# Kernel optimization log

Hardware: AMD Instinct MI355X
Metric: run time of the kernel (lower is better)

## Reference

```python
import jax, jax.numpy as jnp
import numpy as np

SMOOTH = 1.0
MAX_DIST = 10


def _neighbor_conv(x):
    # 3x3 ones kernel with zero center, padding=1 (NCHW, C=1)
    k = jnp.ones((1, 1, 3, 3), x.dtype).at[0, 0, 1, 1].set(0.0)
    return jax.lax.conv_general_dilated(
        x, k, window_strides=(1, 1), padding=[(1, 1), (1, 1)],
        dimension_numbers=('NCHW', 'OIHW', 'NCHW'))


def _analyze_skeleton(skel):
    n = _neighbor_conv(skel)
    on = skel > 0.5
    endpoints = ((n == 1) & on).astype(skel.dtype)
    midpoints = ((n == 2) & on).astype(skel.dtype)
    junctions = ((n > 2) & on).astype(skel.dtype)
    return endpoints, midpoints, junctions


def _iou(p, g):
    inter = jnp.sum(p * g, axis=(2, 3))
    union = jnp.sum(p, axis=(2, 3)) + jnp.sum(g, axis=(2, 3)) - inter
    return (inter + SMOOTH) / (union + SMOOTH)


def _structural_similarity(pred_skel, gt_skel):
    pe, pm, pj = _analyze_skeleton(pred_skel)
    ge, gm, gj = _analyze_skeleton(gt_skel)
    e_iou, m_iou, j_iou = _iou(pe, ge), _iou(pm, gm), _iou(pj, gj)
    ge_c = jnp.sum(ge, axis=(2, 3))
    gj_c = jnp.sum(gj, axis=(2, 3))
    gm_c = jnp.sum(gm, axis=(2, 3))
    total = ge_c + gj_c + gm_c + SMOOTH
    loss = 1.0 - ((ge_c / total) * e_iou + (gj_c / total) * j_iou + (gm_c / total) * m_iou)
    return loss.mean()


def _maxpool3(x):
    return jax.lax.reduce_window(
        x, -jnp.inf, jax.lax.max,
        window_dimensions=(1, 1, 3, 3), window_strides=(1, 1, 1, 1),
        padding=[(0, 0), (0, 0), (1, 1), (1, 1)])


def _distance_approximation(target, reference):
    # Fixed MAX_DIST iterations; identical math to the torch early-exit loop
    # because new_points requires ~found_mask (no distance is overwritten).
    tgt_on = target > 0.5

    def step(carry, d):
        dilated, found, dist = carry
        dilated = _maxpool3(dilated)
        new = (dilated > 0.5) & tgt_on & (~found)
        dist = dist + d.astype(dist.dtype) * new.astype(dist.dtype)
        return (dilated, found | new, dist), None

    init = (reference, jnp.zeros(target.shape, bool), jnp.zeros_like(target))
    (_, found, dist), _ = jax.lax.scan(step, init, jnp.arange(1, MAX_DIST + 1, dtype=jnp.int32))
    unfound = tgt_on & (~found)
    dist = dist + jnp.asarray(MAX_DIST, dist.dtype) * unfound.astype(dist.dtype)
    total_points = jnp.sum(tgt_on.astype(dist.dtype), axis=(2, 3))
    return jnp.sum(dist, axis=(2, 3)) / (total_points + SMOOTH)


def _medial_axis_distance(pred_skel, gt_skel):
    p2g = _distance_approximation(pred_skel, gt_skel)
    g2p = _distance_approximation(gt_skel, pred_skel)
    return (((p2g + g2p) / 2.0) / MAX_DIST).mean()


def setup_inputs() -> dict:
    key = jax.random.key(0)
    k1, k2 = jax.random.split(key)
    B, C, H, W = 32, 1, 512, 512
    pred_skel = jax.random.uniform(k1, (B, C, H, W), dtype=jnp.float32)
    gt_skel = (jax.random.uniform(k2, (B, C, H, W), dtype=jnp.float32) < 0.1).astype(jnp.float32)
    return {"pred_skel": pred_skel, "gt_skel": gt_skel}


def reference(pred_skel, gt_skel):
    inter = jnp.sum(pred_skel * gt_skel, axis=(2, 3))
    psum = jnp.sum(pred_skel, axis=(2, 3))
    gsum = jnp.sum(gt_skel, axis=(2, 3))
    dice = (2.0 * inter + SMOOTH) / (psum + gsum + SMOOTH)
    dice_loss = 1.0 - dice.mean()
    structural_loss = _structural_similarity(pred_skel, gt_skel)
    medial_loss = _medial_axis_distance(pred_skel, gt_skel)
    avg_mag = (dice_loss + structural_loss + medial_loss) / 3.0
    bal_dice = dice_loss / (dice_loss + SMOOTH) * avg_mag
    bal_struct = structural_loss / (structural_loss + SMOOTH) * avg_mag
    bal_medial = medial_loss / (medial_loss + SMOOTH) * avg_mag
    return bal_dice + bal_struct + bal_medial
```

## Files before the change

### kernel.cpp

```cpp
#include <hip/hip_runtime.h>
#include <stdint.h>

#define BATCH 32
#define H 512
#define W 512
#define NACC 16
#define TH 32
#define HALO 9
#define RH (TH + 2*HALO)
#define NWORDS (RH*8)
#define NT 512
#define NW (NT/64)
#define NTILE (H/TH)
#define NBLK (NTILE*BATCH)


__global__ __launch_bounds__(NT, 4) void fused_kernel(
    const float* __restrict__ pred, const float* __restrict__ gt,
    float* __restrict__ part)
{
    __shared__ uint64_t MpS[NWORDS + 2];
    __shared__ uint64_t MgS[NWORDS + 2];
    __shared__ float    EC[2][TH];
    __shared__ float    red[NW][16];

    uint64_t* Mp = MpS + 1;
    uint64_t* Mg = MgS + 1;

    int fid  = blockIdx.x;
    int b    = fid & 31;
    int tile = fid >> 5;

    const float* pimg = pred + (size_t)b * H * W;
    const float* gimg = gt   + (size_t)b * H * W;
    int y0 = tile * TH;
    int tid = threadIdx.x, lane = tid & 63, wid = tid >> 6;

    for (int s = wid; s < NWORDS; s += 2 * NW) {
        int sB = s + NW;
        int ryA = y0 - HALO + (s >> 3);
        int ryB = y0 - HALO + (sB >> 3);
        float vpA = 0.f, vgA = 0.f, vpB = 0.f, vgB = 0.f;
        if ((unsigned)ryA < (unsigned)H) {
            int i0 = ryA * W + (s & 7) * 64 + lane;
            vpA = pimg[i0]; vgA = gimg[i0];
        }
        if ((unsigned)ryB < (unsigned)H) {
            int i1 = ryB * W + (sB & 7) * 64 + lane;
            vpB = pimg[i1]; vgB = gimg[i1];
        }
        unsigned long long mpA = __ballot(vpA > 0.5f);
        unsigned long long mgA = __ballot(vgA > 0.5f);
        unsigned long long mpB = __ballot(vpB > 0.5f);
        unsigned long long mgB = __ballot(vgB > 0.5f);
        if (lane == 0) {
            Mp[s]  = mpA; Mg[s]  = mgA;
            Mp[sB] = mpB; Mg[sB] = mgB;
        }
    }
    if (tid == 0) { MpS[0] = 0; MpS[NWORDS + 1] = 0; MgS[0] = 0; MgS[NWORDS + 1] = 0; }
    if (tid < 2 * TH) {
        int c = tid >> 5, r = tid & (TH - 1);
        int y = y0 + r, col = 255 + c;
        float sum = (y > 0     ? pimg[(size_t)(y - 1) * W + col] : 0.f)
                  +              pimg[(size_t)y * W + col]
                  + (y < H - 1 ? pimg[(size_t)(y + 1) * W + col] : 0.f);
        EC[c][r] = sum;
    }
    __syncthreads();

    float v0 = 0.f, v1 = 0.f;
    uint64_t cpack = 0ULL;
    {
        int qi = tid & 127, h = tid >> 7;
        int x4 = qi * 4;
        int wdx = qi >> 4;
        int ss = (qi & 15) * 4;
        int ys = y0 + h * 8;

        auto win6 = [&](int rb) -> uint32_t {
            const uint64_t* row = &Mg[rb * 8];
            uint64_t bm = row[wdx];
            if (ss == 0) {
                uint64_t lo = wdx ? row[wdx - 1] : 0ULL;
                return (uint32_t)(((bm << 1) | (lo >> 63)) & 0x3FULL);
            }
            uint32_t v = (uint32_t)((bm >> (ss - 1)) & 0x3FULL);
            if (ss == 60) {
                uint64_t hi = (wdx < 7) ? row[wdx + 1] : 0ULL;
                v |= ((uint32_t)hi & 1u) << 5;
            }
            return v;
        };

        int rb0 = h * 8 + HALO - 1;
        uint32_t wU = win6(rb0), wM = win6(rb0 + 1);

        float4 pm4, pc4;
        {
            bool hm = ys > 0;
            pm4 = hm ? *(const float4*)(pimg + (size_t)(ys - 1) * W + x4)
                     : make_float4(0, 0, 0, 0);
            pc4 = *(const float4*)(pimg + (size_t)ys * W + x4);
        }
        for (int r = 0; r < 8; ++r) {
            int y = ys + r;
            float4 pp4 = (y < H - 1) ? *(const float4*)(pimg + (size_t)(y + 1) * W + x4)
                                     : make_float4(0, 0, 0, 0);
            uint32_t wD = win6(rb0 + 2 + r);
            int ry = h * 8 + r;

            float ps[6];
            ps[1] = pm4.x + pc4.x + pp4.x; ps[2] = pm4.y + pc4.y + pp4.y;
            ps[3] = pm4.z + pc4.z + pp4.z; ps[4] = pm4.w + pc4.w + pp4.w;
            float psl = __shfl_up(ps[4], 1, 64);
            float psr = __shfl_down(ps[1], 1, 64);
            if (lane == 0)  psl = (qi == 0)   ? 0.f : EC[0][ry];
            if (lane == 63) psr = (qi == 127) ? 0.f : EC[1][ry];
            ps[0] = psl; ps[5] = psr;

            float pcv[4] = {pc4.x, pc4.y, pc4.z, pc4.w};
            #pragma unroll
            for (int j = 0; j < 4; ++j) {
                float np = ps[j] + ps[j + 1] + ps[j + 2] - pcv[j];
                bool pon = pcv[j] > 0.5f;
                bool pe  = pon && (np == 1.f);
                bool pmb = pon && (np == 2.f);
                bool pjb = pon && (np > 2.f);
                uint32_t n9 = ((wU >> j) & 7u) | (((wM >> j) & 7u) << 3) | (((wD >> j) & 7u) << 6);
                uint32_t cen = (wM >> (j + 1)) & 1u;
                int ng = __popc(n9) - (int)cen;
                bool gon = cen != 0u;
                bool ge  = gon && (ng == 1);
                bool gmb = gon && (ng == 2);
                bool gjb = gon && (ng > 2);
                v1 += pcv[j];
                v0 += gon ? pcv[j] : 0.f;
                cpack += (uint64_t)pe
                       | ((uint64_t)pmb << 7)
                       | ((uint64_t)pjb << 14)
                       | ((uint64_t)ge  << 21)
                       | ((uint64_t)gmb << 28)
                       | ((uint64_t)gjb << 35)
                       | ((uint64_t)(pe  && ge)  << 42)
                       | ((uint64_t)(pmb && gmb) << 49)
                       | ((uint64_t)(pjb && gjb) << 56);
            }
            pm4 = pc4; pc4 = pp4; wU = wM; wM = wD;
        }
    }

    bool isP = tid < 256;
    int idx = tid & 255;
    int o   = (HALO + (idx >> 3)) * 8 + (idx & 7);
    int w   = idx & 7;
    bool wL = (w > 0), wR = (w < 7);
    const uint64_t* MT = isP ? Mp : Mg;
    const uint64_t* MV = isP ? Mg : Mp;

    uint64_t T = MT[o];
    int dcnt = __popcll(T);
    int dsum = dcnt;
    uint64_t VM = MV[o];
    uint64_t VL = wL ? MV[o - 1] : 0ULL;
    uint64_t VR = wR ? MV[o + 1] : 0ULL;
    uint64_t C = VM;

    #pragma unroll
    for (int a = 1; a <= 9; ++a) {
        int lo = o - 8 * a, hi = o + 8 * a;
        uint64_t NM = MV[lo] | MV[hi];
        uint64_t NL = wL ? (MV[lo - 1] | MV[hi - 1]) : 0ULL;
        uint64_t NR = wR ? (MV[lo + 1] | MV[hi + 1]) : 0ULL;
        uint64_t SL = NL, SM = NM, SR = NR;
        const int m = a - 1;
        if (m >= 1) {
            SM |= (SM << 1) | (SM >> 1) | (SL >> 63) | (SR << 63);
            SL |= SL << 1; SR |= SR >> 1;
        }
        if (m >= 2) {
            const int s = (m == 2) ? 1 : 2;
            SM |= (SM << s) | (SM >> s) | (SL >> (64 - s)) | (SR << (64 - s));
            SL |= SL << s; SR |= SR >> s;
        }
        if (m >= 4) {
            const int s = (m - 3 < 4) ? (m - 3) : 4;
            SM |= (SM << s) | (SM >> s) | (SL >> (64 - s)) | (SR << (64 - s));
            SL |= SL << s; SR |= SR >> s;
        }
        if (m >= 8) {
            const int s = m - 7;
            SM |= (SM << s) | (SM >> s) | (SL >> (64 - s)) | (SR << (64 - s));
            SL |= SL << s; SR |= SR >> s;
        }
        C |= SM;
        VL |= NL; VM |= NM; VR |= NR;
        C |= (VM << a) | (VM >> a) | (VL >> (64 - a)) | (VR << (64 - a));
        dsum += __popcll(T & ~C);
    }

    float vals[16];
    vals[0] = v0; vals[1] = v1;
    vals[2]  = isP ? 0.f : (float)dcnt;
    vals[3]  = (float)((cpack      ) & 0x7F);
    vals[4]  = (float)((cpack >> 7 ) & 0x7F);
    vals[5]  = (float)((cpack >> 14) & 0x7F);
    vals[6]  = (float)((cpack >> 21) & 0x7F);
    vals[7]  = (float)((cpack >> 28) & 0x7F);
    vals[8]  = (float)((cpack >> 35) & 0x7F);
    vals[9]  = (float)((cpack >> 42) & 0x7F);
    vals[10] = (float)((cpack >> 49) & 0x7F);
    vals[11] = (float)((cpack >> 56) & 0x7F);
    vals[12] = isP ? (float)dsum : 0.f;
    vals[13] = isP ? (float)dcnt : 0.f;
    vals[14] = isP ? 0.f : (float)dsum;
    vals[15] = isP ? 0.f : (float)dcnt;
    #pragma unroll
    for (int j = 0; j < 16; ++j)
        #pragma unroll
        for (int off = 32; off; off >>= 1)
            vals[j] += __shfl_down(vals[j], off, 64);
    if (lane == 0) {
        #pragma unroll
        for (int j = 0; j < 16; ++j) red[wid][j] = vals[j];
    }
    __syncthreads();
    if (tid < 16) {
        float s = 0.f;
        #pragma unroll
        for (int wv = 0; wv < NW; ++wv) s += red[wv][tid];
        part[fid * NACC + tid] = s;
    }
}

__global__ __launch_bounds__(512) void final_kernel(
    const float* __restrict__ part, float* __restrict__ out)
{
    __shared__ float sacc[BATCH][NACC];
    __shared__ float tri[BATCH][3];
    int t = threadIdx.x;
    {
        int b = t >> 4, k = t & 15;
        float s = 0.f;
        #pragma unroll 4
        for (int j = 0; j < NTILE; ++j)
            s += part[((j << 5) + b) * NACC + k];
        sacc[b][k] = s;
    }
    __syncthreads();
    if (t < BATCH) {
        const float* a = sacc[t];
        float inter = a[0], psum = a[1], gsum = a[2];
        float dice = (2.f * inter + 1.f) / (psum + gsum + 1.f);

        float pe = a[3], pm = a[4], pj = a[5];
        float ge = a[6], gm = a[7], gj = a[8];
        float ie = a[9], im = a[10], ij = a[11];
        float e_iou = (ie + 1.f) / (pe + ge - ie + 1.f);
        float m_iou = (im + 1.f) / (pm + gm - im + 1.f);
        float j_iou = (ij + 1.f) / (pj + gj - ij + 1.f);
        float total = ge + gj + gm + 1.f;
        float sloss = 1.f - ((ge / total) * e_iou + (gj / total) * j_iou + (gm / total) * m_iou);

        float p2g = a[12] / (a[13] + 1.f);
        float g2p = a[14] / (a[15] + 1.f);
        float med = ((p2g + g2p) * 0.5f) / 10.f;
        tri[t][0] = dice; tri[t][1] = sloss; tri[t][2] = med;
    }
    __syncthreads();
    if (t == 0) {
        float dice = 0.f, sloss = 0.f, med = 0.f;
        for (int b = 0; b < BATCH; ++b) {
            dice += tri[b][0]; sloss += tri[b][1]; med += tri[b][2];
        }
        float dice_loss  = 1.f - dice / (float)BATCH;
        float structural = sloss / (float)BATCH;
        float medial     = med / (float)BATCH;
        float avg = (dice_loss + structural + medial) / 3.f;
        float r = dice_loss  / (dice_loss  + 1.f) * avg
                + structural / (structural + 1.f) * avg
                + medial     / (medial     + 1.f) * avg;
        out[0] = r;
    }
}

extern "C" void kernel_launch(void* const* d_in, const int* in_sizes, int n_in,
                              void* d_out, int out_size, void* d_ws, size_t ws_size,
                              hipStream_t stream)
{
    const float* pred = (const float*)d_in[0];
    const float* gt   = (const float*)d_in[1];
    float* part = (float*)d_ws;
    float* out  = (float*)d_out;

    fused_kernel<<<dim3(NBLK), NT, 0, stream>>>(pred, gt, part);
    final_kernel<<<1, 512, 0, stream>>>(part, out);
}
```

Before: 126.5 us.

## Double block size, split stencil into pre-sync pred pass and post-sync GT pass

Raises threads per block to 1024 so each thread handles 4 rows instead of 8. The pred-neighbour stencil, which only reads global memory, now runs before the barrier, which overlaps it with the shared bitmask build. The dice sums move into the bitmask load loop, and the edge-column sums come from per-lane loads instead of a shared EC array. Flags are packed as 3-bit fields and counted with popcount masks. Only half the threads run the distance loop, and the larger block may cut occupancy and raise register pressure.

Result: slower. 167.9 us (+32.7%).

```diff
diff --git a/kernel.cpp b/kernel.cpp
--- a/kernel.cpp
+++ b/kernel.cpp
@@ -9,7 +9,7 @@
 #define HALO 9
 #define RH (TH + 2*HALO)
 #define NWORDS (RH*8)
-#define NT 512
+#define NT 1024
 #define NW (NT/64)
 #define NTILE (H/TH)
 #define NBLK (NTILE*BATCH)
@@ -21,7 +21,6 @@
 {
     __shared__ uint64_t MpS[NWORDS + 2];
     __shared__ uint64_t MgS[NWORDS + 2];
-    __shared__ float    EC[2][TH];
     __shared__ float    red[NW][16];
 
     uint64_t* Mp = MpS + 1;
@@ -36,48 +35,89 @@
     int y0 = tile * TH;
     int tid = threadIdx.x, lane = tid & 63, wid = tid >> 6;
 
+    float v0 = 0.f, v1 = 0.f;
     for (int s = wid; s < NWORDS; s += 2 * NW) {
         int sB = s + NW;
-        int ryA = y0 - HALO + (s >> 3);
-        int ryB = y0 - HALO + (sB >> 3);
+        bool okB = sB < NWORDS;
+        int rA = s >> 3, rB = sB >> 3;
+        int ryA = y0 - HALO + rA, ryB = y0 - HALO + rB;
         float vpA = 0.f, vgA = 0.f, vpB = 0.f, vgB = 0.f;
         if ((unsigned)ryA < (unsigned)H) {
             int i0 = ryA * W + (s & 7) * 64 + lane;
             vpA = pimg[i0]; vgA = gimg[i0];
         }
-        if ((unsigned)ryB < (unsigned)H) {
+        if (okB && (unsigned)ryB < (unsigned)H) {
             int i1 = ryB * W + (sB & 7) * 64 + lane;
             vpB = pimg[i1]; vgB = gimg[i1];
         }
         unsigned long long mpA = __ballot(vpA > 0.5f);
         unsigned long long mgA = __ballot(vgA > 0.5f);
-        unsigned long long mpB = __ballot(vpB > 0.5f);
-        unsigned long long mgB = __ballot(vgB > 0.5f);
-        if (lane == 0) {
-            Mp[s]  = mpA; Mg[s]  = mgA;
-            Mp[sB] = mpB; Mg[sB] = mgB;
+        if (lane == 0) { Mp[s] = mpA; Mg[s] = mgA; }
+        if (rA >= HALO && rA < HALO + TH) { v1 += vpA; v0 += (vgA > 0.5f) ? vpA : 0.f; }
+        if (okB) {
+            unsigned long long mpB = __ballot(vpB > 0.5f);
+            unsigned long long mgB = __ballot(vgB > 0.5f);
+            if (lane == 0) { Mp[sB] = mpB; Mg[sB] = mgB; }
+            if (rB >= HALO && rB < HALO + TH) { v1 += vpB; v0 += (vgB > 0.5f) ? vpB : 0.f; }
         }
     }
     if (tid == 0) { MpS[0] = 0; MpS[NWORDS + 1] = 0; MgS[0] = 0; MgS[NWORDS + 1] = 0; }
-    if (tid < 2 * TH) {
-        int c = tid >> 5, r = tid & (TH - 1);
-        int y = y0 + r, col = 255 + c;
-        float sum = (y > 0     ? pimg[(size_t)(y - 1) * W + col] : 0.f)
-                  +              pimg[(size_t)y * W + col]
-                  + (y < H - 1 ? pimg[(size_t)(y + 1) * W + col] : 0.f);
-        EC[c][r] = sum;
-    }
-    __syncthreads();
-
-    float v0 = 0.f, v1 = 0.f;
-    uint64_t cpack = 0ULL;
+
+    uint64_t ppack = 0ULL;
     {
         int qi = tid & 127, h = tid >> 7;
         int x4 = qi * 4;
+        int ys = y0 + h * 4;
+        bool needL = (lane == 0)  && (qi == 64);
+        bool needR = (lane == 63) && (qi == 63);
+        bool needE = needL || needR;
+        int ecol = needL ? 255 : 256;
+        float em = 0.f, ec = 0.f;
+        if (needE) {
+            if (ys > 0) em = pimg[(size_t)(ys - 1) * W + ecol];
+            ec = pimg[(size_t)ys * W + ecol];
+        }
+        float4 pm4 = (ys > 0) ? *(const float4*)(pimg + (size_t)(ys - 1) * W + x4)
+                              : make_float4(0, 0, 0, 0);
+        float4 pc4 = *(const float4*)(pimg + (size_t)ys * W + x4);
+        #pragma unroll
+        for (int r = 0; r < 4; ++r) {
+            int y = ys + r;
+            float4 pp4 = (y < H - 1) ? *(const float4*)(pimg + (size_t)(y + 1) * W + x4)
+                                     : make_float4(0, 0, 0, 0);
+            float ep = 0.f;
+            if (needE && y < H - 1) ep = pimg[(size_t)(y + 1) * W + ecol];
+            float ecs = em + ec + ep;
+
+            float ps[6];
+            ps[1] = pm4.x + pc4.x + pp4.x; ps[2] = pm4.y + pc4.y + pp4.y;
+            ps[3] = pm4.z + pc4.z + pp4.z; ps[4] = pm4.w + pc4.w + pp4.w;
+            float psl = __shfl_up(ps[4], 1, 64);
+            float psr = __shfl_down(ps[1], 1, 64);
+            if (lane == 0)  psl = needL ? ecs : 0.f;
+            if (lane == 63) psr = needR ? ecs : 0.f;
+            ps[0] = psl; ps[5] = psr;
+
+            float pcv[4] = {pc4.x, pc4.y, pc4.z, pc4.w};
+            #pragma unroll
+            for (int j = 0; j < 4; ++j) {
+                float np = ps[j] + ps[j + 1] + ps[j + 2] - pcv[j];
+                bool pon = pcv[j] > 0.5f;
+                uint32_t f = (uint32_t)(pon && (np == 1.f))
+                           | ((uint32_t)(pon && (np == 2.f)) << 1)
+                           | ((uint32_t)(pon && (np > 2.f))  << 2);
+                ppack |= (uint64_t)f << (3 * (r * 4 + j));
+            }
+            pm4 = pc4; pc4 = pp4; em = ec; ec = ep;
+        }
+    }
+    __syncthreads();
+
+    uint64_t gpack = 0ULL;
+    {
+        int qi = tid & 127, h = tid >> 7;
         int wdx = qi >> 4;
         int ss = (qi & 15) * 4;
-        int ys = y0 + h * 8;
-
         auto win6 = [&](int rb) -> uint32_t {
             const uint64_t* row = &Mg[rb * 8];
             uint64_t bm = row[wdx];
@@ -92,129 +132,97 @@
             }
             return v;
         };
-
-        int rb0 = h * 8 + HALO - 1;
+        int rb0 = h * 4 + HALO - 1;
         uint32_t wU = win6(rb0), wM = win6(rb0 + 1);
-
-        float4 pm4, pc4;
-        {
-            bool hm = ys > 0;
-            pm4 = hm ? *(const float4*)(pimg + (size_t)(ys - 1) * W + x4)
-                     : make_float4(0, 0, 0, 0);
-            pc4 = *(const float4*)(pimg + (size_t)ys * W + x4);
-        }
-        for (int r = 0; r < 8; ++r) {
-            int y = ys + r;
-            float4 pp4 = (y < H - 1) ? *(const float4*)(pimg + (size_t)(y + 1) * W + x4)
-                                     : make_float4(0, 0, 0, 0);
+        #pragma unroll
+        for (int r = 0; r < 4; ++r) {
             uint32_t wD = win6(rb0 + 2 + r);
-            int ry = h * 8 + r;
-
-            float ps[6];
-            ps[1] = pm4.x + pc4.x + pp4.x; ps[2] = pm4.y + pc4.y + pp4.y;
-            ps[3] = pm4.z + pc4.z + pp4.z; ps[4] = pm4.w + pc4.w + pp4.w;
-            float psl = __shfl_up(ps[4], 1, 64);
-            float psr = __shfl_down(ps[1], 1, 64);
-            if (lane == 0)  psl = (qi == 0)   ? 0.f : EC[0][ry];
-            if (lane == 63) psr = (qi == 127) ? 0.f : EC[1][ry];
-            ps[0] = psl; ps[5] = psr;
-
-            float pcv[4] = {pc4.x, pc4.y, pc4.z, pc4.w};
             #pragma unroll
             for (int j = 0; j < 4; ++j) {
-                float np = ps[j] + ps[j + 1] + ps[j + 2] - pcv[j];
-                bool pon = pcv[j] > 0.5f;
-                bool pe  = pon && (np == 1.f);
-                bool pmb = pon && (np == 2.f);
-                bool pjb = pon && (np > 2.f);
                 uint32_t n9 = ((wU >> j) & 7u) | (((wM >> j) & 7u) << 3) | (((wD >> j) & 7u) << 6);
                 uint32_t cen = (wM >> (j + 1)) & 1u;
                 int ng = __popc(n9) - (int)cen;
-                bool gon = cen != 0u;
-                bool ge  = gon && (ng == 1);
-                bool gmb = gon && (ng == 2);
-                bool gjb = gon && (ng > 2);
-                v1 += pcv[j];
-                v0 += gon ? pcv[j] : 0.f;
-                cpack += (uint64_t)pe
-                       | ((uint64_t)pmb << 7)
-                       | ((uint64_t)pjb << 14)
-                       | ((uint64_t)ge  << 21)
-                       | ((uint64_t)gmb << 28)
-                       | ((uint64_t)gjb << 35)
-                       | ((uint64_t)(pe  && ge)  << 42)
-                       | ((uint64_t)(pmb && gmb) << 49)
-                       | ((uint64_t)(pjb && gjb) << 56);
-            }
-            pm4 = pc4; pc4 = pp4; wU = wM; wM = wD;
-        }
-    }
-
-    bool isP = tid < 256;
-    int idx = tid & 255;
-    int o   = (HALO + (idx >> 3)) * 8 + (idx & 7);
-    int w   = idx & 7;
-    bool wL = (w > 0), wR = (w < 7);
-    const uint64_t* MT = isP ? Mp : Mg;
-    const uint64_t* MV = isP ? Mg : Mp;
-
-    uint64_t T = MT[o];
-    int dcnt = __popcll(T);
-    int dsum = dcnt;
-    uint64_t VM = MV[o];
-    uint64_t VL = wL ? MV[o - 1] : 0ULL;
-    uint64_t VR = wR ? MV[o + 1] : 0ULL;
-    uint64_t C = VM;
-
-    #pragma unroll
-    for (int a = 1; a <= 9; ++a) {
-        int lo = o - 8 * a, hi = o + 8 * a;
-        uint64_t NM = MV[lo] | MV[hi];
-        uint64_t NL = wL ? (MV[lo - 1] | MV[hi - 1]) : 0ULL;
-        uint64_t NR = wR ? (MV[lo + 1] | MV[hi + 1]) : 0ULL;
-        uint64_t SL = NL, SM = NM, SR = NR;
-        const int m = a - 1;
-        if (m >= 1) {
-            SM |= (SM << 1) | (SM >> 1) | (SL >> 63) | (SR << 63);
-            SL |= SL << 1; SR |= SR >> 1;
-        }
-        if (m >= 2) {
-            const int s = (m == 2) ? 1 : 2;
-            SM |= (SM << s) | (SM >> s) | (SL >> (64 - s)) | (SR << (64 - s));
-            SL |= SL << s; SR |= SR >> s;
-        }
-        if (m >= 4) {
-            const int s = (m - 3 < 4) ? (m - 3) : 4;
-            SM |= (SM << s) | (SM >> s) | (SL >> (64 - s)) | (SR << (64 - s));
-            SL |= SL << s; SR |= SR >> s;
-        }
-        if (m >= 8) {
-            const int s = m - 7;
-            SM |= (SM << s) | (SM >> s) | (SL >> (64 - s)) | (SR << (64 - s));
-            SL |= SL << s; SR |= SR >> s;
-        }
-        C |= SM;
-        VL |= NL; VM |= NM; VR |= NR;
-        C |= (VM << a) | (VM >> a) | (VL >> (64 - a)) | (VR << (64 - a));
-        dsum += __popcll(T & ~C);
+                uint32_t f = cen ? ((uint32_t)(ng == 1)
+                                 | ((uint32_t)(ng == 2) << 1)
+                                 | ((uint32_t)(ng > 2)  << 2)) : 0u;
+                gpack |= (uint64_t)f << (3 * (r * 4 + j));
+            }
+            wU = wM; wM = wD;
+        }
+    }
+    const uint64_t M0 = 0x249249249249ULL;
+    const uint64_t M1 = 0x492492492492ULL;
+    const uint64_t M2 = 0x924924924924ULL;
+    uint64_t ipack = ppack & gpack;
+
+    int dsum_p = 0, dcnt_p = 0, dsum_g = 0, dcnt_g = 0;
+    if (tid < 512) {
+        bool isP = tid < 256;
+        int idx = tid & 255;
+        int o   = (HALO + (idx >> 3)) * 8 + (idx & 7);
+        int w   = idx & 7;
+        bool wL = (w > 0), wR = (w < 7);
+        const uint64_t* MT = isP ? Mp : Mg;
+        const uint64_t* MV = isP ? Mg : Mp;
+
+        uint64_t T = MT[o];
+        int dcnt = __popcll(T);
+        int dsum = dcnt;
+        uint64_t VM = MV[o];
+        uint64_t VL = wL ? MV[o - 1] : 0ULL;
+        uint64_t VR = wR ? MV[o + 1] : 0ULL;
+        uint64_t C = VM;
+
+        #pragma unroll
+        for (int a = 1; a <= 9; ++a) {
+            int lo = o - 8 * a, hi = o + 8 * a;
+            uint64_t NM = MV[lo] | MV[hi];
+            uint64_t NL = wL ? (MV[lo - 1] | MV[hi - 1]) : 0ULL;
+            uint64_t NR = wR ? (MV[lo + 1] | MV[hi + 1]) : 0ULL;
+            uint64_t SL = NL, SM = NM, SR = NR;
+            const int m = a - 1;
+            if (m >= 1) {
+                SM |= (SM << 1) | (SM >> 1) | (SL >> 63) | (SR << 63);
+                SL |= SL << 1; SR |= SR >> 1;
+            }
+            if (m >= 2) {
+                const int s = (m == 2) ? 1 : 2;
+                SM |= (SM << s) | (SM >> s) | (SL >> (64 - s)) | (SR << (64 - s));
+                SL |= SL << s; SR |= SR >> s;
+            }
+            if (m >= 4) {
+                const int s = (m - 3 < 4) ? (m - 3) : 4;
+                SM |= (SM << s) | (SM >> s) | (SL >> (64 - s)) | (SR << (64 - s));
+                SL |= SL << s; SR |= SR >> s;
+            }
+            if (m >= 8) {
+                const int s = m - 7;
+                SM |= (SM << s) | (SM >> s) | (SL >> (64 - s)) | (SR << (64 - s));
+                SL |= SL << s; SR |= SR >> s;
+            }
+            C |= SM;
+            VL |= NL; VM |= NM; VR |= NR;
+            C |= (VM << a) | (VM >> a) | (VL >> (64 - a)) | (VR << (64 - a));
+            dsum += __popcll(T & ~C);
+        }
+        if (isP) { dsum_p = dsum; dcnt_p = dcnt; }
+        else     { dsum_g = dsum; dcnt_g = dcnt; }
     }
 
     float vals[16];
-    vals[0] = v0; vals[1] = v1;
-    vals[2]  = isP ? 0.f : (float)dcnt;
-    vals[3]  = (float)((cpack      ) & 0x7F);
-    vals[4]  = (float)((cpack >> 7 ) & 0x7F);
-    vals[5]  = (float)((cpack >> 14) & 0x7F);
-    vals[6]  = (float)((cpack >> 21) & 0x7F);
-    vals[7]  = (float)((cpack >> 28) & 0x7F);
-    vals[8]  = (float)((cpack >> 35) & 0x7F);
-    vals[9]  = (float)((cpack >> 42) & 0x7F);
-    vals[10] = (float)((cpack >> 49) & 0x7F);
-    vals[11] = (float)((cpack >> 56) & 0x7F);
-    vals[12] = isP ? (float)dsum : 0.f;
-    vals[13] = isP ? (float)dcnt : 0.f;
-    vals[14] = isP ? 0.f : (float)dsum;
-    vals[15] = isP ? 0.f : (float)dcnt;
+    vals[0]  = v0; vals[1] = v1;
+    vals[2]  = (float)dcnt_g;
+    vals[3]  = (float)__popcll(ppack & M0);
+    vals[4]  = (float)__popcll(ppack & M1);
+    vals[5]  = (float)__popcll(ppack & M2);
+    vals[6]  = (float)__popcll(gpack & M0);
+    vals[7]  = (float)__popcll(gpack & M1);
+    vals[8]  = (float)__popcll(gpack & M2);
+    vals[9]  = (float)__popcll(ipack & M0);
+    vals[10] = (float)__popcll(ipack & M1);
+    vals[11] = (float)__popcll(ipack & M2);
+    vals[12] = (float)dsum_p; vals[13] = (float)dcnt_p;
+    vals[14] = (float)dsum_g; vals[15] = (float)dcnt_g;
     #pragma unroll
     for (int j = 0; j < 16; ++j)
         #pragma unroll
```

## Split block into stencil and distance warp groups with packed integer reduction

Applied to the files above, without the earlier changes.

Doubles the block to 1024 threads so the 3x3 neighbor-classification stencil and the bit-mask distance dilation run concurrently on separate warp halves instead of serially on the same threads. The dice sums move into the mask-building loop, and the loads are batched four rows at a time. The 16-float shuffle reduction is replaced by 7 values, with integer counts packed two per 32-bit word. This trades more warps per block for launch_bounds occupancy pressure: 1024 threads with a min of 4 blocks may force register spilling. It also adds divergence between the two roles.

Result: faster. 117.7 us (-7.0%).

```diff
diff --git a/kernel.cpp b/kernel.cpp
--- a/kernel.cpp
+++ b/kernel.cpp
@@ -9,7 +9,7 @@
 #define HALO 9
 #define RH (TH + 2*HALO)
 #define NWORDS (RH*8)
-#define NT 512
+#define NT 1024
 #define NW (NT/64)
 #define NTILE (H/TH)
 #define NBLK (NTILE*BATCH)
@@ -22,7 +22,8 @@
     __shared__ uint64_t MpS[NWORDS + 2];
     __shared__ uint64_t MgS[NWORDS + 2];
     __shared__ float    EC[2][TH];
-    __shared__ float    red[NW][16];
+    __shared__ float    redf[NW][2];
+    __shared__ unsigned redu[NW][5];
 
     uint64_t* Mp = MpS + 1;
     uint64_t* Mg = MgS + 1;
@@ -36,29 +37,47 @@
     int y0 = tile * TH;
     int tid = threadIdx.x, lane = tid & 63, wid = tid >> 6;
 
-    for (int s = wid; s < NWORDS; s += 2 * NW) {
-        int sB = s + NW;
-        int ryA = y0 - HALO + (s >> 3);
-        int ryB = y0 - HALO + (sB >> 3);
-        float vpA = 0.f, vgA = 0.f, vpB = 0.f, vgB = 0.f;
-        if ((unsigned)ryA < (unsigned)H) {
-            int i0 = ryA * W + (s & 7) * 64 + lane;
-            vpA = pimg[i0]; vgA = gimg[i0];
-        }
-        if ((unsigned)ryB < (unsigned)H) {
-            int i1 = ryB * W + (sB & 7) * 64 + lane;
-            vpB = pimg[i1]; vgB = gimg[i1];
-        }
-        unsigned long long mpA = __ballot(vpA > 0.5f);
-        unsigned long long mgA = __ballot(vgA > 0.5f);
-        unsigned long long mpB = __ballot(vpB > 0.5f);
-        unsigned long long mgB = __ballot(vgB > 0.5f);
-        if (lane == 0) {
-            Mp[s]  = mpA; Mg[s]  = mgA;
-            Mp[sB] = mpB; Mg[sB] = mgB;
+    float v0 = 0.f, v1 = 0.f;
+    for (int s0 = wid; s0 < NWORDS; s0 += 4 * NW) {
+        float vp[4], vg[4];
+        #pragma unroll
+        for (int u = 0; u < 4; ++u) {
+            int s = s0 + u * NW;
+            vp[u] = 0.f; vg[u] = 0.f;
+            int ry = y0 - HALO + (s >> 3);
+            if (s < NWORDS && (unsigned)ry < (unsigned)H) {
+                int i0 = ry * W + (s & 7) * 64 + lane;
+                vp[u] = pimg[i0]; vg[u] = gimg[i0];
+            }
+        }
+        #pragma unroll
+        for (int u = 0; u < 4; ++u) {
+            int s = s0 + u * NW;
+            if (s < NWORDS) {
+                unsigned long long mp = __ballot(vp[u] > 0.5f);
+                unsigned long long mg = __ballot(vg[u] > 0.5f);
+                if (lane == 0) { Mp[s] = mp; Mg[s] = mg; }
+                int r = s >> 3;
+                if (r >= HALO && r < HALO + TH) {
+                    v1 += vp[u];
+                    v0 += (vg[u] > 0.5f) ? vp[u] : 0.f;
+                }
+            }
         }
     }
     if (tid == 0) { MpS[0] = 0; MpS[NWORDS + 1] = 0; MgS[0] = 0; MgS[NWORDS + 1] = 0; }
+
+    bool isStencil = tid >= 512;
+    int idx = tid & 511;
+    int qi = idx & 127, h2 = idx >> 7;
+    int x4 = qi * 4;
+    int ys = y0 + h2 * 8;
+    float4 pm4 = make_float4(0, 0, 0, 0), pc4 = make_float4(0, 0, 0, 0);
+    if (isStencil) {
+        if (ys > 0) pm4 = *(const float4*)(pimg + (size_t)(ys - 1) * W + x4);
+        pc4 = *(const float4*)(pimg + (size_t)ys * W + x4);
+    }
+
     if (tid < 2 * TH) {
         int c = tid >> 5, r = tid & (TH - 1);
         int y = y0 + r, col = 255 + c;
@@ -69,15 +88,12 @@
     }
     __syncthreads();
 
-    float v0 = 0.f, v1 = 0.f;
     uint64_t cpack = 0ULL;
-    {
-        int qi = tid & 127, h = tid >> 7;
-        int x4 = qi * 4;
+    int dsum = 0, dcnt = 0;
+
+    if (isStencil) {
         int wdx = qi >> 4;
         int ss = (qi & 15) * 4;
-        int ys = y0 + h * 8;
-
         auto win6 = [&](int rb) -> uint32_t {
             const uint64_t* row = &Mg[rb * 8];
             uint64_t bm = row[wdx];
@@ -92,23 +108,15 @@
             }
             return v;
         };
-
-        int rb0 = h * 8 + HALO - 1;
+        int rb0 = h2 * 8 + HALO - 1;
         uint32_t wU = win6(rb0), wM = win6(rb0 + 1);
 
-        float4 pm4, pc4;
-        {
-            bool hm = ys > 0;
-            pm4 = hm ? *(const float4*)(pimg + (size_t)(ys - 1) * W + x4)
-                     : make_float4(0, 0, 0, 0);
-            pc4 = *(const float4*)(pimg + (size_t)ys * W + x4);
-        }
         for (int r = 0; r < 8; ++r) {
             int y = ys + r;
             float4 pp4 = (y < H - 1) ? *(const float4*)(pimg + (size_t)(y + 1) * W + x4)
                                      : make_float4(0, 0, 0, 0);
             uint32_t wD = win6(rb0 + 2 + r);
-            int ry = h * 8 + r;
+            int ry = h2 * 8 + r;
 
             float ps[6];
             ps[1] = pm4.x + pc4.x + pp4.x; ps[2] = pm4.y + pc4.y + pp4.y;
@@ -134,8 +142,6 @@
                 bool ge  = gon && (ng == 1);
                 bool gmb = gon && (ng == 2);
                 bool gjb = gon && (ng > 2);
-                v1 += pcv[j];
-                v0 += gon ? pcv[j] : 0.f;
                 cpack += (uint64_t)pe
                        | ((uint64_t)pmb << 7)
                        | ((uint64_t)pjb << 14)
@@ -148,88 +154,117 @@
             }
             pm4 = pc4; pc4 = pp4; wU = wM; wM = wD;
         }
-    }
-
-    bool isP = tid < 256;
-    int idx = tid & 255;
-    int o   = (HALO + (idx >> 3)) * 8 + (idx & 7);
-    int w   = idx & 7;
-    bool wL = (w > 0), wR = (w < 7);
-    const uint64_t* MT = isP ? Mp : Mg;
-    const uint64_t* MV = isP ? Mg : Mp;
-
-    uint64_t T = MT[o];
-    int dcnt = __popcll(T);
-    int dsum = dcnt;
-    uint64_t VM = MV[o];
-    uint64_t VL = wL ? MV[o - 1] : 0ULL;
-    uint64_t VR = wR ? MV[o + 1] : 0ULL;
-    uint64_t C = VM;
-
+    } else {
+        bool isP = tid < 256;
+        int di = tid & 255;
+        int o  = (HALO + (di >> 3)) * 8 + (di & 7);
+        int w  = di & 7;
+        bool wL = (w > 0), wR = (w < 7);
+        const uint64_t* MT = isP ? Mp : Mg;
+        const uint64_t* MV = isP ? Mg : Mp;
+
+        uint64_t T = MT[o];
+        dcnt = __popcll(T);
+        dsum = dcnt;
+        uint64_t VM = MV[o];
+        uint64_t VL = wL ? MV[o - 1] : 0ULL;
+        uint64_t VR = wR ? MV[o + 1] : 0ULL;
+        uint64_t C = VM;
+
+        #pragma unroll
+        for (int a = 1; a <= 9; ++a) {
+            int lo = o - 8 * a, hi = o + 8 * a;
+            uint64_t NM = MV[lo] | MV[hi];
+            uint64_t NL = wL ? (MV[lo - 1] | MV[hi - 1]) : 0ULL;
+            uint64_t NR = wR ? (MV[lo + 1] | MV[hi + 1]) : 0ULL;
+            uint64_t SL = NL, SM = NM, SR = NR;
+            const int m = a - 1;
+            if (m >= 1) {
+                SM |= (SM << 1) | (SM >> 1) | (SL >> 63) | (SR << 63);
+                SL |= SL << 1; SR |= SR >> 1;
+            }
+            if (m >= 2) {
+                const int s = (m == 2) ? 1 : 2;
+                SM |= (SM << s) | (SM >> s) | (SL >> (64 - s)) | (SR << (64 - s));
+                SL |= SL << s; SR |= SR >> s;
+            }
+            if (m >= 4) {
+                const int s = (m - 3 < 4) ? (m - 3) : 4;
+                SM |= (SM << s) | (SM >> s) | (SL >> (64 - s)) | (SR << (64 - s));
+                SL |= SL << s; SR |= SR >> s;
+            }
+            if (m >= 8) {
+                const int s = m - 7;
+                SM |= (SM << s) | (SM >> s) | (SL >> (64 - s)) | (SR << (64 - s));
+                SL |= SL << s; SR |= SR >> s;
+            }
+            C |= SM;
+            VL |= NL; VM |= NM; VR |= NR;
+            C |= (VM << a) | (VM >> a) | (VL >> (64 - a)) | (VR << (64 - a));
+            dsum += __popcll(T & ~C);
+        }
+    }
+
+    unsigned r0, r1, r2, r3, r4;
+    if (isStencil) {
+        unsigned c3  = (unsigned)( cpack        & 0x7F);
+        unsigned c4  = (unsigned)((cpack >> 7 ) & 0x7F);
+        unsigned c5  = (unsigned)((cpack >> 14) & 0x7F);
+        unsigned c6  = (unsigned)((cpack >> 21) & 0x7F);
+        unsigned c7  = (unsigned)((cpack >> 28) & 0x7F);
+        unsigned c8  = (unsigned)((cpack >> 35) & 0x7F);
+        unsigned c9  = (unsigned)((cpack >> 42) & 0x7F);
+        unsigned c10 = (unsigned)((cpack >> 49) & 0x7F);
+        unsigned c11 = (unsigned)((cpack >> 56) & 0x7F);
+        r0 = c3 | (c4 << 16); r1 = c5 | (c6 << 16); r2 = c7 | (c8 << 16);
+        r3 = c9 | (c10 << 16); r4 = c11;
+    } else {
+        r0 = (unsigned)dsum | ((unsigned)dcnt << 16);
+        r1 = 0; r2 = 0; r3 = 0; r4 = 0;
+    }
     #pragma unroll
-    for (int a = 1; a <= 9; ++a) {
-        int lo = o - 8 * a, hi = o + 8 * a;
-        uint64_t NM = MV[lo] | MV[hi];
-        uint64_t NL = wL ? (MV[lo - 1] | MV[hi - 1]) : 0ULL;
-        uint64_t NR = wR ? (MV[lo + 1] | MV[hi + 1]) : 0ULL;
-        uint64_t SL = NL, SM = NM, SR = NR;
-        const int m = a - 1;
-        if (m >= 1) {
-            SM |= (SM << 1) | (SM >> 1) | (SL >> 63) | (SR << 63);
-            SL |= SL << 1; SR |= SR >> 1;
-        }
-        if (m >= 2) {
-            const int s = (m == 2) ? 1 : 2;
-            SM |= (SM << s) | (SM >> s) | (SL >> (64 - s)) | (SR << (64 - s));
-            SL |= SL << s; SR |= SR >> s;
-        }
-        if (m >= 4) {
-            const int s = (m - 3 < 4) ? (m - 3) : 4;
-            SM |= (SM << s) | (SM >> s) | (SL >> (64 - s)) | (SR << (64 - s));
-            SL |= SL << s; SR |= SR >> s;
-        }
-        if (m >= 8) {
-            const int s = m - 7;
-            SM |= (SM << s) | (SM >> s) | (SL >> (64 - s)) | (SR << (64 - s));
-            SL |= SL << s; SR |= SR >> s;
-        }
-        C |= SM;
-        VL |= NL; VM |= NM; VR |= NR;
-        C |= (VM << a) | (VM >> a) | (VL >> (64 - a)) | (VR << (64 - a));
-        dsum += __popcll(T & ~C);
-    }
-
-    float vals[16];
-    vals[0] = v0; vals[1] = v1;
-    vals[2]  = isP ? 0.f : (float)dcnt;
-    vals[3]  = (float)((cpack      ) & 0x7F);
-    vals[4]  = (float)((cpack >> 7 ) & 0x7F);
-    vals[5]  = (float)((cpack >> 14) & 0x7F);
-    vals[6]  = (float)((cpack >> 21) & 0x7F);
-    vals[7]  = (float)((cpack >> 28) & 0x7F);
-    vals[8]  = (float)((cpack >> 35) & 0x7F);
-    vals[9]  = (float)((cpack >> 42) & 0x7F);
-    vals[10] = (float)((cpack >> 49) & 0x7F);
-    vals[11] = (float)((cpack >> 56) & 0x7F);
-    vals[12] = isP ? (float)dsum : 0.f;
-    vals[13] = isP ? (float)dcnt : 0.f;
-    vals[14] = isP ? 0.f : (float)dsum;
-    vals[15] = isP ? 0.f : (float)dcnt;
-    #pragma unroll
-    for (int j = 0; j < 16; ++j)
-        #pragma unroll
-        for (int off = 32; off; off >>= 1)
-            vals[j] += __shfl_down(vals[j], off, 64);
+    for (int off = 32; off; off >>= 1) {
+        v0 += __shfl_down(v0, off, 64);
+        v1 += __shfl_down(v1, off, 64);
+        r0 += __shfl_down(r0, off, 64);
+        r1 += __shfl_down(r1, off, 64);
+        r2 += __shfl_down(r2, off, 64);
+        r3 += __shfl_down(r3, off, 64);
+        r4 += __shfl_down(r4, off, 64);
+    }
     if (lane == 0) {
-        #pragma unroll
-        for (int j = 0; j < 16; ++j) red[wid][j] = vals[j];
+        redf[wid][0] = v0; redf[wid][1] = v1;
+        redu[wid][0] = r0; redu[wid][1] = r1; redu[wid][2] = r2;
+        redu[wid][3] = r3; redu[wid][4] = r4;
     }
     __syncthreads();
     if (tid < 16) {
+        int k = tid;
         float s = 0.f;
-        #pragma unroll
-        for (int wv = 0; wv < NW; ++wv) s += red[wv][tid];
-        part[fid * NACC + tid] = s;
+        if (k < 2) {
+            #pragma unroll
+            for (int wv = 0; wv < NW; ++wv) s += redf[wv][k];
+        } else if (k == 2) {
+            unsigned u = 0;
+            for (int wv = 4; wv < 8; ++wv) u += redu[wv][0] >> 16;
+            s = (float)u;
+        } else if (k <= 10) {
+            int pair = (k - 3) >> 1, hi = (k - 3) & 1;
+            unsigned u = 0;
+            for (int wv = 8; wv < 16; ++wv) u += (redu[wv][pair] >> (hi * 16)) & 0xFFFFu;
+            s = (float)u;
+        } else if (k == 11) {
+            unsigned u = 0;
+            for (int wv = 8; wv < 16; ++wv) u += redu[wv][4];
+            s = (float)u;
+        } else {
+            int base = (k < 14) ? 0 : 4, hi = k & 1;
+            unsigned u = 0;
+            for (int wv = base; wv < base + 4; ++wv)
+                u += (redu[wv][0] >> (hi * 16)) & 0xFFFFu;
+            s = (float)u;
+        }
+        part[fid * NACC + k] = s;
     }
 }
 
```
